# Kernel tuning notes

Measured on AMD Instinct MI355X. Metric: run time of the kernel, lower is better.

Reference implementation:

```python
import jax, jax.numpy as jnp
import numpy as np

N = 100000   # nodes
E = 1600000  # edges
D = 128      # input feature dim
H = 64       # hidden dim
G = 64       # graphs in batch


def setup_inputs() -> dict:
    key = jax.random.key(0)
    ks = jax.random.split(key, 12)
    x = jax.random.normal(ks[0], (N, D), dtype=jnp.float32)
    ei = jax.random.randint(ks[1], (2, E), 0, N, dtype=jnp.int32)
    ew = jax.random.uniform(ks[2], (E,), dtype=jnp.float32)
    b = jnp.sort(jax.random.randint(ks[3], (N,), 0, G, dtype=jnp.int32))
    s = 0.05
    W1 = jax.random.normal(ks[4], (D, H), jnp.float32) * s
    b1 = jnp.zeros((H,), jnp.float32)
    W2 = jax.random.normal(ks[5], (H, H), jnp.float32) * s
    b2 = jnp.zeros((H,), jnp.float32)
    Wm1 = jax.random.normal(ks[6], (H, 32), jnp.float32) * s
    bm1 = jnp.zeros((32,), jnp.float32)
    Wm2 = jax.random.normal(ks[7], (32, 1), jnp.float32) * s
    bm2 = jnp.zeros((1,), jnp.float32)
    return {"x": x, "ei": ei, "ew": ew, "b": b,
            "W1": W1, "b1": b1, "W2": W2, "b2": b2,
            "Wm1": Wm1, "bm1": bm1, "Wm2": Wm2, "bm2": bm2}


def _gcn_norm(ei, ew, n):
    # PyG gcn_norm with add_self_loops=True (self-loop weight 1)
    loops = jnp.arange(n, dtype=ei.dtype)
    row = jnp.concatenate([ei[0], loops])
    col = jnp.concatenate([ei[1], loops])
    w = jnp.concatenate([ew, jnp.ones((n,), ew.dtype)])
    deg = jax.ops.segment_sum(w, col, num_segments=n)
    dinv = jnp.where(deg > 0, jax.lax.rsqrt(deg), 0.0)
    norm = dinv[row] * w * dinv[col]  # [E+N]
    return row, col, norm


def _gcn_conv(x, W, bias, row, col, norm, n):
    h = x @ W                                   # [N,H] small GEMM
    msg = h[row] * norm[:, None]                # gather over edges
    return jax.ops.segment_sum(msg, col, num_segments=n) + bias


def reference(x, ei, ew, b, W1, b1, W2, b2, Wm1, bm1, Wm2, bm2):
    n = x.shape[0]
    row, col, norm = _gcn_norm(ei, ew, n)
    h = jax.nn.relu(_gcn_conv(x, W1, b1, row, col, norm, n))
    h = jax.nn.relu(_gcn_conv(h, W2, b2, row, col, norm, n))
    # global_mean_pool over batch vector b
    sums = jax.ops.segment_sum(h, b, num_segments=G)
    cnt = jax.ops.segment_sum(jnp.ones((n,), h.dtype), b, num_segments=G)
    pooled = sums / jnp.maximum(cnt, 1.0)[:, None]  # [G,H]
    # MLP head: Linear(H,32) -> ReLU -> Linear(32,1)
    return jax.nn.relu(pooled @ Wm1 + bm1) @ Wm2 + bm2
```

## Files before the change

### kernel.cpp

```cpp
#include <hip/hip_runtime.h>
#include <hip/hip_bf16.h>
#include <hip/hip_fp16.h>


#define DIMH 64
#define BSH 7
#define BSZ 128
#define NBUCK_MAX 1024
#define EPB 4096
#define ESTRIDE 3072
#define CSTRIDE 4096

typedef _Float16 v8h __attribute__((ext_vector_type(8)));
typedef _Float16 v4h __attribute__((ext_vector_type(4)));
typedef _Float16 hv2 __attribute__((ext_vector_type(2)));
typedef float v4f __attribute__((ext_vector_type(4)));

__global__ __launch_bounds__(512) void k_part(const int* __restrict__ row,
                                              const int* __restrict__ col,
                                              const float* __restrict__ ew,
                                              int* __restrict__ cursor,
                                              unsigned long long* __restrict__ part,
                                              int E, int nbuck) {
    __shared__ int h[NBUCK_MAX];
    __shared__ int h2[NBUCK_MAX];
    __shared__ int st[NBUCK_MAX];
    for (int i = threadIdx.x; i < nbuck; i += 512) { h[i] = 0; h2[i] = 0; }
    __syncthreads();
    int ebeg = blockIdx.x * EPB;
    int eend = min(ebeg + EPB, E);
    int myc[8];
    int m = 0;
    for (int e = ebeg + threadIdx.x; e < eend; e += 512) {
        int c = col[e];
        myc[m++] = c;
        atomicAdd(&h[c >> BSH], 1);
    }
    __syncthreads();
    for (int i = threadIdx.x; i < nbuck; i += 512) {
        int c = h[i];
        st[i] = c ? i * ESTRIDE + atomicAdd(&cursor[i], c) : 0;
    }
    __syncthreads();
    m = 0;
    for (int e = ebeg + threadIdx.x; e < eend; e += 512, m++) {
        int c = myc[m];
        int b = c >> BSH;
        int r = atomicAdd(&h2[b], 1);
        int slot = st[b] + r;
        if (slot < (b + 1) * ESTRIDE) {
            unsigned long long rec =
                ((unsigned long long)__float_as_uint(ew[e]) << 32) |
                ((unsigned long long)(unsigned)row[e] << 8) |
                (unsigned)(c & (BSZ - 1));
            part[slot] = rec;
        }
    }
}

__global__ __launch_bounds__(256) void k_sortB(const unsigned long long* __restrict__ part,
                                               const int* __restrict__ cursor,
                                               int2* __restrict__ csr,
                                               unsigned* __restrict__ rp,
                                               float* __restrict__ dinv, int N) {
    __shared__ int cnt[BSZ];
    __shared__ int scn[BSZ];
    __shared__ int cur[BSZ];
    __shared__ float dg[BSZ];
    int b = blockIdx.x;
    int nb0 = b << BSH;
    int nn = min(BSZ, N - nb0);
    int tid = threadIdx.x;
    if (tid < BSZ) { cnt[tid] = 0; dg[tid] = 1.0f; }
    __syncthreads();
    int ebeg = b * ESTRIDE;
    int eend = ebeg + min(cursor[b], ESTRIDE);
    unsigned long long myrec[12];
    int nrec = 0;
    for (int e = ebeg + tid; e < eend; e += 256) {
        unsigned long long rec = part[e];
        myrec[nrec++] = rec;
        atomicAdd(&cnt[(int)(rec & (BSZ - 1))], 1);
    }
    __syncthreads();
    int pc = 0;
    if (tid < BSZ) pc = min((cnt[tid] + 7) & ~7, 496);
    if (tid < BSZ) scn[tid] = pc;
    __syncthreads();
    for (int o = 1; o < BSZ; o <<= 1) {
        int t = 0;
        if (tid >= o && tid < BSZ) t = scn[tid - o];
        __syncthreads();
        if (tid >= o && tid < BSZ) scn[tid] += t;
        __syncthreads();
    }
    int Pb = b * CSTRIDE;
    int pofs = 0;
    if (tid < BSZ) {
        pofs = scn[tid] - pc;
        cur[tid] = pofs;
        if (tid < nn)
            rp[nb0 + tid] = ((unsigned)(pc >> 3) << 26) | (unsigned)(Pb + pofs);
    }
    __syncthreads();
    for (int i = 0; i < nrec; i++) {
        unsigned long long rec = myrec[i];
        int cl = (int)(rec & (BSZ - 1));
        float w = __uint_as_float((unsigned)(rec >> 32));
        int slot = atomicAdd(&cur[cl], 1);
        csr[Pb + slot] = make_int2((int)((rec >> 8) & 0xFFFFFF), __float_as_int(w));
        atomicAdd(&dg[cl], w);
    }
    __syncthreads();
    if (tid < nn) {
        int c = min(cnt[tid], pc);
        for (int k = c; k < pc; k++)
            csr[Pb + pofs + k] = make_int2(nb0 + tid, 0);
        dinv[nb0 + tid] = rsqrtf(dg[tid]);
    }
}

__global__ __launch_bounds__(256) void k_gemm_mfma(const float* __restrict__ X,
                                                   const float* __restrict__ W,
                                                   const float* __restrict__ dinv,
                                                   __half* __restrict__ Y, int n) {
    __shared__ _Float16 Wh[128 * 64];
    int tid = threadIdx.x;
    for (int i = tid * 4; i < 128 * 64; i += 256 * 4) {
        float4 w = *(const float4*)&W[i];
        Wh[i]     = (_Float16)w.x;
        Wh[i + 1] = (_Float16)w.y;
        Wh[i + 2] = (_Float16)w.z;
        Wh[i + 3] = (_Float16)w.w;
    }
    __syncthreads();

    int wv = tid >> 6;
    int lane = tid & 63;
    int m = lane & 15;
    int quad = lane >> 4;
    int tile = blockIdx.x * 4 + wv;
    int ntiles = (n + 15) >> 4;
    if (tile >= ntiles) return;

    v8h bf[4][4];
#pragma unroll
    for (int nt = 0; nt < 4; nt++)
#pragma unroll
        for (int s = 0; s < 4; s++)
#pragma unroll
            for (int j = 0; j < 8; j++)
                bf[nt][s][j] = Wh[(s * 32 + quad * 8 + j) * 64 + nt * 16 + m];

    v4f acc[4];
#pragma unroll
    for (int nt = 0; nt < 4; nt++) acc[nt] = (v4f){0.f, 0.f, 0.f, 0.f};

    int row = min(tile * 16 + m, n - 1);
    const float* xr = X + (size_t)row * 128;
#pragma unroll
    for (int s = 0; s < 4; s++) {
        float4 lo = *(const float4*)&xr[s * 32 + quad * 8];
        float4 hi = *(const float4*)&xr[s * 32 + quad * 8 + 4];
        v8h af;
        af[0] = (_Float16)lo.x; af[1] = (_Float16)lo.y;
        af[2] = (_Float16)lo.z; af[3] = (_Float16)lo.w;
        af[4] = (_Float16)hi.x; af[5] = (_Float16)hi.y;
        af[6] = (_Float16)hi.z; af[7] = (_Float16)hi.w;
#pragma unroll
        for (int nt = 0; nt < 4; nt++)
            acc[nt] = __builtin_amdgcn_mfma_f32_16x16x32_f16(af, bf[nt][s], acc[nt], 0, 0, 0);
    }

#pragma unroll
    for (int r = 0; r < 4; r++) {
        int node = tile * 16 + quad * 4 + r;
        if (node < n) {
            float di = dinv[node];
#pragma unroll
            for (int nt = 0; nt < 4; nt++)
                Y[(size_t)node * DIMH + nt * 16 + m] = __float2half(di * acc[nt][r]);
        }
    }
}

__global__ __launch_bounds__(256, 8) void k_agg1f(const __half* __restrict__ Hin,
                                                  const unsigned* __restrict__ rp,
                                                  const int2* __restrict__ csr,
                                                  const float* __restrict__ dinv,
                                                  const float* __restrict__ bias,
                                                  const float* __restrict__ W2,
                                                  __half* __restrict__ T2, int n) {
    __shared__ __align__(16) _Float16 W2T[64 * 68];
    __shared__ __align__(16) _Float16 hbuf[4][DIMH];
    int tid = threadIdx.x;
    for (int idx = tid; idx < 64 * 64; idx += 256) {
        int k = idx >> 6;
        int o = idx & 63;
        W2T[o * 68 + k] = (_Float16)W2[idx];
    }
    __syncthreads();

    int lane = tid & 63;
    int wv = tid >> 6;
    int q = lane >> 4;
    int fp = lane & 15;

    const char* Hb = (const char*)Hin;
    const char* Cb = (const char*)csr;
    int ngroups = (n + 3) >> 2;
    for (int grp = blockIdx.x; grp < ngroups; grp += gridDim.x) {
        int node = grp * 4 + wv;
        if (node >= n) continue;
        unsigned pk = rp[node];
        unsigned pb = ((pk & 0x3FFFFFFu) << 3) + (unsigned)(q << 4);
        int g8 = (int)(pk >> 26);
        float a0 = 0.f, a1 = 0.f, a2 = 0.f, a3 = 0.f;
        if (q == 0) {
            uint2 su = *(const uint2*)(Hb + (((unsigned)node << 7) + (unsigned)(fp << 3)));
            float2 f0 = __half22float2(*(__half2*)&su.x);
            float2 f1 = __half22float2(*(__half2*)&su.y);
            a0 = f0.x; a1 = f0.y; a2 = f1.x; a3 = f1.y;
        }
        unsigned fo = (unsigned)(fp << 3);
        int it = 0;
        for (; it + 4 <= g8; it += 4, pb += 256) {
            int4 mA0 = *(const int4*)(Cb + pb);
            int4 mB0 = *(const int4*)(Cb + pb + 64);
            int4 mA1 = *(const int4*)(Cb + pb + 128);
            int4 mB1 = *(const int4*)(Cb + pb + 192);
            uint2 u0 = *(const uint2*)(Hb + (((unsigned)mA0.x << 7) + fo));
            uint2 u1 = *(const uint2*)(Hb + (((unsigned)mA0.z << 7) + fo));
            uint2 u2 = *(const uint2*)(Hb + (((unsigned)mB0.x << 7) + fo));
            uint2 u3 = *(const uint2*)(Hb + (((unsigned)mB0.z << 7) + fo));
            uint2 u4 = *(const uint2*)(Hb + (((unsigned)mA1.x << 7) + fo));
            uint2 u5 = *(const uint2*)(Hb + (((unsigned)mA1.z << 7) + fo));
            uint2 u6 = *(const uint2*)(Hb + (((unsigned)mB1.x << 7) + fo));
            uint2 u7 = *(const uint2*)(Hb + (((unsigned)mB1.z << 7) + fo));
            float w0 = __int_as_float(mA0.y), w1 = __int_as_float(mA0.w);
            float w2 = __int_as_float(mB0.y), w3 = __int_as_float(mB0.w);
            float w4 = __int_as_float(mA1.y), w5 = __int_as_float(mA1.w);
            float w6 = __int_as_float(mB1.y), w7 = __int_as_float(mB1.w);
            float2 f;
            f = __half22float2(*(__half2*)&u0.x); a0 += w0 * f.x; a1 += w0 * f.y;
            f = __half22float2(*(__half2*)&u0.y); a2 += w0 * f.x; a3 += w0 * f.y;
            f = __half22float2(*(__half2*)&u1.x); a0 += w1 * f.x; a1 += w1 * f.y;
            f = __half22float2(*(__half2*)&u1.y); a2 += w1 * f.x; a3 += w1 * f.y;
            f = __half22float2(*(__half2*)&u2.x); a0 += w2 * f.x; a1 += w2 * f.y;
            f = __half22float2(*(__half2*)&u2.y); a2 += w2 * f.x; a3 += w2 * f.y;
            f = __half22float2(*(__half2*)&u3.x); a0 += w3 * f.x; a1 += w3 * f.y;
            f = __half22float2(*(__half2*)&u3.y); a2 += w3 * f.x; a3 += w3 * f.y;
            f = __half22float2(*(__half2*)&u4.x); a0 += w4 * f.x; a1 += w4 * f.y;
            f = __half22float2(*(__half2*)&u4.y); a2 += w4 * f.x; a3 += w4 * f.y;
            f = __half22float2(*(__half2*)&u5.x); a0 += w5 * f.x; a1 += w5 * f.y;
            f = __half22float2(*(__half2*)&u5.y); a2 += w5 * f.x; a3 += w5 * f.y;
            f = __half22float2(*(__half2*)&u6.x); a0 += w6 * f.x; a1 += w6 * f.y;
            f = __half22float2(*(__half2*)&u6.y); a2 += w6 * f.x; a3 += w6 * f.y;
            f = __half22float2(*(__half2*)&u7.x); a0 += w7 * f.x; a1 += w7 * f.y;
            f = __half22float2(*(__half2*)&u7.y); a2 += w7 * f.x; a3 += w7 * f.y;
        }
        if (it + 2 <= g8) {
            int4 mA = *(const int4*)(Cb + pb);
            int4 mB = *(const int4*)(Cb + pb + 64);
            uint2 u0 = *(const uint2*)(Hb + (((unsigned)mA.x << 7) + fo));
            uint2 u1 = *(const uint2*)(Hb + (((unsigned)mA.z << 7) + fo));
            uint2 u2 = *(const uint2*)(Hb + (((unsigned)mB.x << 7) + fo));
            uint2 u3 = *(const uint2*)(Hb + (((unsigned)mB.z << 7) + fo));
            float w0 = __int_as_float(mA.y), w1 = __int_as_float(mA.w);
            float w2 = __int_as_float(mB.y), w3 = __int_as_float(mB.w);
            float2 f;
            f = __half22float2(*(__half2*)&u0.x); a0 += w0 * f.x; a1 += w0 * f.y;
            f = __half22float2(*(__half2*)&u0.y); a2 += w0 * f.x; a3 += w0 * f.y;
            f = __half22float2(*(__half2*)&u1.x); a0 += w1 * f.x; a1 += w1 * f.y;
            f = __half22float2(*(__half2*)&u1.y); a2 += w1 * f.x; a3 += w1 * f.y;
            f = __half22float2(*(__half2*)&u2.x); a0 += w2 * f.x; a1 += w2 * f.y;
            f = __half22float2(*(__half2*)&u2.y); a2 += w2 * f.x; a3 += w2 * f.y;
            f = __half22float2(*(__half2*)&u3.x); a0 += w3 * f.x; a1 += w3 * f.y;
            f = __half22float2(*(__half2*)&u3.y); a2 += w3 * f.x; a3 += w3 * f.y;
            pb += 128; it += 2;
        }
        if (it < g8) {
            int4 mA = *(const int4*)(Cb + pb);
            uint2 u0 = *(const uint2*)(Hb + (((unsigned)mA.x << 7) + fo));
            uint2 u1 = *(const uint2*)(Hb + (((unsigned)mA.z << 7) + fo));
            float w0 = __int_as_float(mA.y), w1 = __int_as_float(mA.w);
            float2 f;
            f = __half22float2(*(__half2*)&u0.x); a0 += w0 * f.x; a1 += w0 * f.y;
            f = __half22float2(*(__half2*)&u0.y); a2 += w0 * f.x; a3 += w0 * f.y;
            f = __half22float2(*(__half2*)&u1.x); a0 += w1 * f.x; a1 += w1 * f.y;
            f = __half22float2(*(__half2*)&u1.y); a2 += w1 * f.x; a3 += w1 * f.y;
        }
        a0 += __shfl_xor(a0, 16, 64); a0 += __shfl_xor(a0, 32, 64);
        a1 += __shfl_xor(a1, 16, 64); a1 += __shfl_xor(a1, 32, 64);
        a2 += __shfl_xor(a2, 16, 64); a2 += __shfl_xor(a2, 32, 64);
        a3 += __shfl_xor(a3, 16, 64); a3 += __shfl_xor(a3, 32, 64);
        float di = dinv[node];
        if (q == 0) {
            float4 bs = *(const float4*)&bias[fp * 4];
            float v0 = fmaxf(di * a0 + bs.x, 0.f);
            float v1 = fmaxf(di * a1 + bs.y, 0.f);
            float v2 = fmaxf(di * a2 + bs.z, 0.f);
            float v3 = fmaxf(di * a3 + bs.w, 0.f);
            __half2 h0 = __floats2half2_rn(v0, v1);
            __half2 h1 = __floats2half2_rn(v2, v3);
            uint2 o;
            o.x = *(unsigned*)&h0;
            o.y = *(unsigned*)&h1;
            *(uint2*)&hbuf[wv][fp * 4] = o;
        }
        float accA = 0.f, accB = 0.f;
#pragma unroll
        for (int k8 = 0; k8 < 8; k8++) {
            v8h hv = *(const v8h*)&hbuf[wv][k8 * 8];
            v4h wa = *(const v4h*)&W2T[lane * 68 + k8 * 8];
            v4h wb = *(const v4h*)&W2T[lane * 68 + k8 * 8 + 4];
            hv2 h0 = {hv[0], hv[1]}, h1 = {hv[2], hv[3]};
            hv2 h2_ = {hv[4], hv[5]}, h3 = {hv[6], hv[7]};
            hv2 w0 = {wa[0], wa[1]}, w1 = {wa[2], wa[3]};
            hv2 w2_ = {wb[0], wb[1]}, w3 = {wb[2], wb[3]};
            accA = __builtin_amdgcn_fdot2(h0, w0, accA, false);
            accB = __builtin_amdgcn_fdot2(h1, w1, accB, false);
            accA = __builtin_amdgcn_fdot2(h2_, w2_, accA, false);
            accB = __builtin_amdgcn_fdot2(h3, w3, accB, false);
        }
        T2[(size_t)node * DIMH + lane] = __float2half(di * (accA + accB));
    }
}

__global__ __launch_bounds__(256, 8) void k_aggN(const __half* __restrict__ Hin,
                                                 const unsigned* __restrict__ rp,
                                                 const int2* __restrict__ csr,
                                                 const float* __restrict__ dinv,
                                                 const float* __restrict__ bias,
                                                 __half* __restrict__ Hout, int n) {
    int lane = threadIdx.x & 63;
    int wv = threadIdx.x >> 6;
    int node = blockIdx.x * 4 + wv;
    if (node >= n) return;
    unsigned pk = rp[node];
    int g8 = (int)(pk >> 26);
    int q = lane >> 4;
    int fp = lane & 15;
    unsigned pb = ((pk & 0x3FFFFFFu) << 3) + (unsigned)(q << 4);
    unsigned fo = (unsigned)(fp << 3);
    const char* Hb = (const char*)Hin;
    const char* Cb = (const char*)csr;
    float a0 = 0.f, a1 = 0.f, a2 = 0.f, a3 = 0.f;
    if (q == 0) {
        uint2 su = *(const uint2*)(Hb + (((unsigned)node << 7) + fo));
        float2 f0 = __half22float2(*(__half2*)&su.x);
        float2 f1 = __half22float2(*(__half2*)&su.y);
        a0 = f0.x; a1 = f0.y; a2 = f1.x; a3 = f1.y;
    }
    int it = 0;
    for (; it + 4 <= g8; it += 4, pb += 256) {
        int4 mA0 = *(const int4*)(Cb + pb);
        int4 mB0 = *(const int4*)(Cb + pb + 64);
        int4 mA1 = *(const int4*)(Cb + pb + 128);
        int4 mB1 = *(const int4*)(Cb + pb + 192);
        uint2 u0 = *(const uint2*)(Hb + (((unsigned)mA0.x << 7) + fo));
        uint2 u1 = *(const uint2*)(Hb + (((unsigned)mA0.z << 7) + fo));
        uint2 u2 = *(const uint2*)(Hb + (((unsigned)mB0.x << 7) + fo));
        uint2 u3 = *(const uint2*)(Hb + (((unsigned)mB0.z << 7) + fo));
        uint2 u4 = *(const uint2*)(Hb + (((unsigned)mA1.x << 7) + fo));
        uint2 u5 = *(const uint2*)(Hb + (((unsigned)mA1.z << 7) + fo));
        uint2 u6 = *(const uint2*)(Hb + (((unsigned)mB1.x << 7) + fo));
        uint2 u7 = *(const uint2*)(Hb + (((unsigned)mB1.z << 7) + fo));
        float w0 = __int_as_float(mA0.y), w1 = __int_as_float(mA0.w);
        float w2 = __int_as_float(mB0.y), w3 = __int_as_float(mB0.w);
        float w4 = __int_as_float(mA1.y), w5 = __int_as_float(mA1.w);
        float w6 = __int_as_float(mB1.y), w7 = __int_as_float(mB1.w);
        float2 f;
        f = __half22float2(*(__half2*)&u0.x); a0 += w0 * f.x; a1 += w0 * f.y;
        f = __half22float2(*(__half2*)&u0.y); a2 += w0 * f.x; a3 += w0 * f.y;
        f = __half22float2(*(__half2*)&u1.x); a0 += w1 * f.x; a1 += w1 * f.y;
        f = __half22float2(*(__half2*)&u1.y); a2 += w1 * f.x; a3 += w1 * f.y;
        f = __half22float2(*(__half2*)&u2.x); a0 += w2 * f.x; a1 += w2 * f.y;
        f = __half22float2(*(__half2*)&u2.y); a2 += w2 * f.x; a3 += w2 * f.y;
        f = __half22float2(*(__half2*)&u3.x); a0 += w3 * f.x; a1 += w3 * f.y;
        f = __half22float2(*(__half2*)&u3.y); a2 += w3 * f.x; a3 += w3 * f.y;
        f = __half22float2(*(__half2*)&u4.x); a0 += w4 * f.x; a1 += w4 * f.y;
        f = __half22float2(*(__half2*)&u4.y); a2 += w4 * f.x; a3 += w4 * f.y;
        f = __half22float2(*(__half2*)&u5.x); a0 += w5 * f.x; a1 += w5 * f.y;
        f = __half22float2(*(__half2*)&u5.y); a2 += w5 * f.x; a3 += w5 * f.y;
        f = __half22float2(*(__half2*)&u6.x); a0 += w6 * f.x; a1 += w6 * f.y;
        f = __half22float2(*(__half2*)&u6.y); a2 += w6 * f.x; a3 += w6 * f.y;
        f = __half22float2(*(__half2*)&u7.x); a0 += w7 * f.x; a1 += w7 * f.y;
        f = __half22float2(*(__half2*)&u7.y); a2 += w7 * f.x; a3 += w7 * f.y;
    }
    if (it + 2 <= g8) {
        int4 mA = *(const int4*)(Cb + pb);
        int4 mB = *(const int4*)(Cb + pb + 64);
        uint2 u0 = *(const uint2*)(Hb + (((unsigned)mA.x << 7) + fo));
        uint2 u1 = *(const uint2*)(Hb + (((unsigned)mA.z << 7) + fo));
        uint2 u2 = *(const uint2*)(Hb + (((unsigned)mB.x << 7) + fo));
        uint2 u3 = *(const uint2*)(Hb + (((unsigned)mB.z << 7) + fo));
        float w0 = __int_as_float(mA.y), w1 = __int_as_float(mA.w);
        float w2 = __int_as_float(mB.y), w3 = __int_as_float(mB.w);
        float2 f;
        f = __half22float2(*(__half2*)&u0.x); a0 += w0 * f.x; a1 += w0 * f.y;
        f = __half22float2(*(__half2*)&u0.y); a2 += w0 * f.x; a3 += w0 * f.y;
        f = __half22float2(*(__half2*)&u1.x); a0 += w1 * f.x; a1 += w1 * f.y;
        f = __half22float2(*(__half2*)&u1.y); a2 += w1 * f.x; a3 += w1 * f.y;
        f = __half22float2(*(__half2*)&u2.x); a0 += w2 * f.x; a1 += w2 * f.y;
        f = __half22float2(*(__half2*)&u2.y); a2 += w2 * f.x; a3 += w2 * f.y;
        f = __half22float2(*(__half2*)&u3.x); a0 += w3 * f.x; a1 += w3 * f.y;
        f = __half22float2(*(__half2*)&u3.y); a2 += w3 * f.x; a3 += w3 * f.y;
        pb += 128; it += 2;
    }
    if (it < g8) {
        int4 mA = *(const int4*)(Cb + pb);
        uint2 u0 = *(const uint2*)(Hb + (((unsigned)mA.x << 7) + fo));
        uint2 u1 = *(const uint2*)(Hb + (((unsigned)mA.z << 7) + fo));
        float w0 = __int_as_float(mA.y), w1 = __int_as_float(mA.w);
        float2 f;
        f = __half22float2(*(__half2*)&u0.x); a0 += w0 * f.x; a1 += w0 * f.y;
        f = __half22float2(*(__half2*)&u0.y); a2 += w0 * f.x; a3 += w0 * f.y;
        f = __half22float2(*(__half2*)&u1.x); a0 += w1 * f.x; a1 += w1 * f.y;
        f = __half22float2(*(__half2*)&u1.y); a2 += w1 * f.x; a3 += w1 * f.y;
    }
    a0 += __shfl_xor(a0, 16, 64); a0 += __shfl_xor(a0, 32, 64);
    a1 += __shfl_xor(a1, 16, 64); a1 += __shfl_xor(a1, 32, 64);
    a2 += __shfl_xor(a2, 16, 64); a2 += __shfl_xor(a2, 32, 64);
    a3 += __shfl_xor(a3, 16, 64); a3 += __shfl_xor(a3, 32, 64);
    if (q == 0) {
        float di = dinv[node];
        float4 bs = *(const float4*)&bias[fp * 4];
        float v0 = fmaxf(di * a0 + bs.x, 0.f);
        float v1 = fmaxf(di * a1 + bs.y, 0.f);
        float v2 = fmaxf(di * a2 + bs.z, 0.f);
        float v3 = fmaxf(di * a3 + bs.w, 0.f);
        __half2 h0 = __floats2half2_rn(v0, v1);
        __half2 h1 = __floats2half2_rn(v2, v3);
        uint2 o;
        o.x = *(unsigned*)&h0;
        o.y = *(unsigned*)&h1;
        *(uint2*)&Hout[(size_t)node * DIMH + fp * 4] = o;
    }
}

__global__ __launch_bounds__(256) void k_pool(const __half* __restrict__ Hin,
                                              const int* __restrict__ b,
                                              float* __restrict__ sums,
                                              float* __restrict__ cntG, int n) {
    const int CHUNK = 64;
    int lane = threadIdx.x & 63;
    int wave = threadIdx.x >> 6;
    int start = (blockIdx.x * 4 + wave) * CHUNK;
    if (start >= n) return;
    int end = min(start + CHUNK, n);
    float acc = 0.f;
    int g_cur = b[start];
    int cnt_local = 0;
    for (int i = start; i < end; i++) {
        int g = b[i];
        if (g != g_cur) {
            atomicAdd(&sums[g_cur * DIMH + lane], acc);
            if (lane == 0) atomicAdd(&cntG[g_cur], (float)cnt_local);
            acc = 0.f;
            cnt_local = 0;
            g_cur = g;
        }
        acc += __half2float(Hin[(size_t)i * DIMH + lane]);
        cnt_local++;
    }
    atomicAdd(&sums[g_cur * DIMH + lane], acc);
    if (lane == 0) atomicAdd(&cntG[g_cur], (float)cnt_local);
}

__global__ __launch_bounds__(64) void k_mlp(const float* __restrict__ sums,
                                            const float* __restrict__ cntG,
                                            const float* __restrict__ Wm1,
                                            const float* __restrict__ bm1,
                                            const float* __restrict__ Wm2,
                                            const float* __restrict__ bm2,
                                            float* __restrict__ out, int G) {
    int g = threadIdx.x;
    if (g >= G) return;
    float c = cntG[g];
    float inv = 1.f / (c > 1.f ? c : 1.f);
    float pooled[DIMH];
#pragma unroll
    for (int k = 0; k < DIMH; k++) pooled[k] = sums[g * DIMH + k] * inv;
    float o = 0.f;
    for (int j = 0; j < 32; j++) {
        float t = bm1[j];
#pragma unroll
        for (int k = 0; k < DIMH; k++) t += pooled[k] * Wm1[k * 32 + j];
        t = t > 0.f ? t : 0.f;
        o += t * Wm2[j];
    }
    out[g] = o + bm2[0];
}


extern "C" void kernel_launch(void* const* d_in, const int* in_sizes, int n_in,
                              void* d_out, int out_size, void* d_ws, size_t ws_size,
                              hipStream_t stream) {
    const float* x   = (const float*)d_in[0];
    const int*   ei  = (const int*)d_in[1];
    const float* ew  = (const float*)d_in[2];
    const int*   bvec= (const int*)d_in[3];
    const float* W1  = (const float*)d_in[4];
    const float* b1  = (const float*)d_in[5];
    const float* W2  = (const float*)d_in[6];
    const float* b2  = (const float*)d_in[7];
    const float* Wm1 = (const float*)d_in[8];
    const float* bm1 = (const float*)d_in[9];
    const float* Wm2 = (const float*)d_in[10];
    const float* bm2 = (const float*)d_in[11];
    float* out = (float*)d_out;

    const int E = in_sizes[2];
    const int N = in_sizes[3];
    const int G = out_size;
    const int* row = ei;
    const int* col = ei + E;
    const int nbuck = (N + BSZ - 1) >> BSH;

    char* p = (char*)d_ws;
    auto alloc = [&](size_t bytes) {
        void* r = (void*)p;
        p += (bytes + 255) & ~(size_t)255;
        return r;
    };

    unsigned long long* part = (unsigned long long*)alloc((size_t)nbuck * ESTRIDE * 8);
    int2*  csr    = (int2*)alloc((size_t)nbuck * CSTRIDE * 8);
    unsigned* rp  = (unsigned*)alloc((size_t)N * 4);
    float* dinv   = (float*)alloc((size_t)N * 4);
    __half* hA    = (__half*)alloc((size_t)N * DIMH * 2);
    __half* hB    = (__half*)alloc((size_t)N * DIMH * 2);
    int zeroInts  = nbuck + G * DIMH + G;
    int* cursor   = (int*)alloc((size_t)zeroInts * 4);
    float* sums   = (float*)(cursor + nbuck);
    float* cntG   = sums + G * DIMH;

    hipMemsetAsync(cursor, 0, (size_t)zeroInts * 4, stream);

    const int PB = (E + EPB - 1) / EPB;
    const int NT = (N + 15) / 16;

    k_part<<<PB, 512, 0, stream>>>(row, col, ew, cursor, part, E, nbuck);
    k_sortB<<<nbuck, 256, 0, stream>>>(part, cursor, csr, rp, dinv, N);

    k_gemm_mfma<<<(NT + 3) / 4, 256, 0, stream>>>(x, W1, dinv, hA, N);

    k_agg1f<<<4096, 256, 0, stream>>>(hA, rp, csr, dinv, b1, W2, hB, N);

    k_aggN<<<(N + 3) / 4, 256, 0, stream>>>(hB, rp, csr, dinv, b2, hA, N);

    k_pool<<<(N + 255) / 256, 256, 0, stream>>>(hA, bvec, sums, cntG, N);
    k_mlp<<<1, 64, 0, stream>>>(sums, cntG, Wm1, bm1, Wm2, bm2, out, G);
}
```

Measured before the change: 307.1 us.

## Replace bucket-partition CSR build with global atomic count, scan, scatter

The two-pass bucket partition (shared-memory histograms, intermediate 64-bit record buffer, per-bucket local sort) is replaced by three kernels. One counts per-node in-degree and weighted degree with global atomics, one does a per-bucket prefix scan that writes row pointers, dinv and padding, and one scatters edges directly into the CSR using per-node atomic cursors. This drops the intermediate partition buffer and its extra read and write pass. In exchange it adds heavy global atomic traffic on random column indices (two atomics per edge in counting, one per edge in scatter) and makes the in-row edge order nondeterministic.

```diff
diff --git a/kernel.cpp b/kernel.cpp
--- a/kernel.cpp
+++ b/kernel.cpp
@@ -6,9 +6,6 @@
 #define DIMH 64
 #define BSH 7
 #define BSZ 128
-#define NBUCK_MAX 1024
-#define EPB 4096
-#define ESTRIDE 3072
 #define CSTRIDE 4096
 
 typedef _Float16 v8h __attribute__((ext_vector_type(8)));
@@ -16,107 +13,102 @@
 typedef _Float16 hv2 __attribute__((ext_vector_type(2)));
 typedef float v4f __attribute__((ext_vector_type(4)));
 
-__global__ __launch_bounds__(512) void k_part(const int* __restrict__ row,
-                                              const int* __restrict__ col,
-                                              const float* __restrict__ ew,
-                                              int* __restrict__ cursor,
-                                              unsigned long long* __restrict__ part,
-                                              int E, int nbuck) {
-    __shared__ int h[NBUCK_MAX];
-    __shared__ int h2[NBUCK_MAX];
-    __shared__ int st[NBUCK_MAX];
-    for (int i = threadIdx.x; i < nbuck; i += 512) { h[i] = 0; h2[i] = 0; }
-    __syncthreads();
-    int ebeg = blockIdx.x * EPB;
-    int eend = min(ebeg + EPB, E);
-    int myc[8];
-    int m = 0;
-    for (int e = ebeg + threadIdx.x; e < eend; e += 512) {
-        int c = col[e];
-        myc[m++] = c;
-        atomicAdd(&h[c >> BSH], 1);
-    }
-    __syncthreads();
-    for (int i = threadIdx.x; i < nbuck; i += 512) {
-        int c = h[i];
-        st[i] = c ? i * ESTRIDE + atomicAdd(&cursor[i], c) : 0;
-    }
-    __syncthreads();
-    m = 0;
-    for (int e = ebeg + threadIdx.x; e < eend; e += 512, m++) {
-        int c = myc[m];
-        int b = c >> BSH;
-        int r = atomicAdd(&h2[b], 1);
-        int slot = st[b] + r;
-        if (slot < (b + 1) * ESTRIDE) {
-            unsigned long long rec =
-                ((unsigned long long)__float_as_uint(ew[e]) << 32) |
-                ((unsigned long long)(unsigned)row[e] << 8) |
-                (unsigned)(c & (BSZ - 1));
-            part[slot] = rec;
-        }
-    }
-}
-
-__global__ __launch_bounds__(256) void k_sortB(const unsigned long long* __restrict__ part,
-                                               const int* __restrict__ cursor,
-                                               int2* __restrict__ csr,
-                                               unsigned* __restrict__ rp,
-                                               float* __restrict__ dinv, int N) {
-    __shared__ int cnt[BSZ];
+__global__ __launch_bounds__(256) void k_count(const int* __restrict__ col,
+                                               const float* __restrict__ ew,
+                                               int* __restrict__ degcnt,
+                                               float* __restrict__ degw, int E) {
+    int i = blockIdx.x * 256 + threadIdx.x;
+    int stride = gridDim.x * 256;
+    int E4 = E >> 2;
+    for (int e = i; e < E4; e += stride) {
+        int4 c = *(const int4*)&col[e * 4];
+        float4 w = *(const float4*)&ew[e * 4];
+        atomicAdd(&degcnt[c.x], 1); atomicAdd(&degw[c.x], w.x);
+        atomicAdd(&degcnt[c.y], 1); atomicAdd(&degw[c.y], w.y);
+        atomicAdd(&degcnt[c.z], 1); atomicAdd(&degw[c.z], w.z);
+        atomicAdd(&degcnt[c.w], 1); atomicAdd(&degw[c.w], w.w);
+    }
+    for (int e = (E4 << 2) + i; e < E; e += stride) {
+        atomicAdd(&degcnt[col[e]], 1);
+        atomicAdd(&degw[col[e]], ew[e]);
+    }
+}
+
+__global__ __launch_bounds__(128) void k_scan(int* __restrict__ degcnt,
+                                              const float* __restrict__ degw,
+                                              int2* __restrict__ csr,
+                                              unsigned* __restrict__ rp,
+                                              float* __restrict__ dinv, int N) {
     __shared__ int scn[BSZ];
-    __shared__ int cur[BSZ];
-    __shared__ float dg[BSZ];
     int b = blockIdx.x;
-    int nb0 = b << BSH;
-    int nn = min(BSZ, N - nb0);
     int tid = threadIdx.x;
-    if (tid < BSZ) { cnt[tid] = 0; dg[tid] = 1.0f; }
-    __syncthreads();
-    int ebeg = b * ESTRIDE;
-    int eend = ebeg + min(cursor[b], ESTRIDE);
-    unsigned long long myrec[12];
-    int nrec = 0;
-    for (int e = ebeg + tid; e < eend; e += 256) {
-        unsigned long long rec = part[e];
-        myrec[nrec++] = rec;
-        atomicAdd(&cnt[(int)(rec & (BSZ - 1))], 1);
-    }
-    __syncthreads();
-    int pc = 0;
-    if (tid < BSZ) pc = min((cnt[tid] + 7) & ~7, 496);
-    if (tid < BSZ) scn[tid] = pc;
+    int node = (b << BSH) + tid;
+    int deg = node < N ? degcnt[node] : 0;
+    int pc = min((deg + 7) & ~7, 496);
+    scn[tid] = pc;
     __syncthreads();
     for (int o = 1; o < BSZ; o <<= 1) {
         int t = 0;
-        if (tid >= o && tid < BSZ) t = scn[tid - o];
+        if (tid >= o) t = scn[tid - o];
         __syncthreads();
-        if (tid >= o && tid < BSZ) scn[tid] += t;
+        if (tid >= o) scn[tid] += t;
         __syncthreads();
     }
-    int Pb = b * CSTRIDE;
-    int pofs = 0;
-    if (tid < BSZ) {
-        pofs = scn[tid] - pc;
-        cur[tid] = pofs;
-        if (tid < nn)
-            rp[nb0 + tid] = ((unsigned)(pc >> 3) << 26) | (unsigned)(Pb + pofs);
-    }
-    __syncthreads();
-    for (int i = 0; i < nrec; i++) {
-        unsigned long long rec = myrec[i];
-        int cl = (int)(rec & (BSZ - 1));
-        float w = __uint_as_float((unsigned)(rec >> 32));
-        int slot = atomicAdd(&cur[cl], 1);
-        csr[Pb + slot] = make_int2((int)((rec >> 8) & 0xFFFFFF), __float_as_int(w));
-        atomicAdd(&dg[cl], w);
-    }
-    __syncthreads();
-    if (tid < nn) {
-        int c = min(cnt[tid], pc);
-        for (int k = c; k < pc; k++)
-            csr[Pb + pofs + k] = make_int2(nb0 + tid, 0);
-        dinv[nb0 + tid] = rsqrtf(dg[tid]);
+    if (node < N) {
+        int pofs = scn[tid] - pc;
+        int Pb = b * CSTRIDE;
+        rp[node] = ((unsigned)(pc >> 3) << 26) | (unsigned)(Pb + pofs);
+        dinv[node] = rsqrtf(1.0f + degw[node]);
+        degcnt[node] = 0;
+        for (int k = deg; k < pc; k++)
+            csr[Pb + pofs + k] = make_int2(node, 0);
+    }
+}
+
+__global__ __launch_bounds__(256) void k_scatter(const int* __restrict__ row,
+                                                 const int* __restrict__ col,
+                                                 const float* __restrict__ ew,
+                                                 const unsigned* __restrict__ rp,
+                                                 int* __restrict__ cur,
+                                                 int2* __restrict__ csr, int E) {
+    int i = blockIdx.x * 256 + threadIdx.x;
+    int stride = gridDim.x * 256;
+    int E4 = E >> 2;
+    for (int e = i; e < E4; e += stride) {
+        int4 r = *(const int4*)&row[e * 4];
+        int4 c = *(const int4*)&col[e * 4];
+        float4 w = *(const float4*)&ew[e * 4];
+        {
+            unsigned pk = rp[c.x];
+            int s = atomicAdd(&cur[c.x], 1);
+            if (s < (int)((pk >> 26) << 3))
+                csr[(pk & 0x3FFFFFFu) + s] = make_int2(r.x, __float_as_int(w.x));
+        }
+        {
+            unsigned pk = rp[c.y];
+            int s = atomicAdd(&cur[c.y], 1);
+            if (s < (int)((pk >> 26) << 3))
+                csr[(pk & 0x3FFFFFFu) + s] = make_int2(r.y, __float_as_int(w.y));
+        }
+        {
+            unsigned pk = rp[c.z];
+            int s = atomicAdd(&cur[c.z], 1);
+            if (s < (int)((pk >> 26) << 3))
+                csr[(pk & 0x3FFFFFFu) + s] = make_int2(r.z, __float_as_int(w.z));
+        }
+        {
+            unsigned pk = rp[c.w];
+            int s = atomicAdd(&cur[c.w], 1);
+            if (s < (int)((pk >> 26) << 3))
+                csr[(pk & 0x3FFFFFFu) + s] = make_int2(r.w, __float_as_int(w.w));
+        }
+    }
+    for (int e = (E4 << 2) + i; e < E; e += stride) {
+        int c = col[e];
+        unsigned pk = rp[c];
+        int s = atomicAdd(&cur[c], 1);
+        if (s < (int)((pk >> 26) << 3))
+            csr[(pk & 0x3FFFFFFu) + s] = make_int2(row[e], __float_as_int(ew[e]));
     }
 }
 
@@ -525,24 +517,25 @@
         return r;
     };
 
-    unsigned long long* part = (unsigned long long*)alloc((size_t)nbuck * ESTRIDE * 8);
     int2*  csr    = (int2*)alloc((size_t)nbuck * CSTRIDE * 8);
     unsigned* rp  = (unsigned*)alloc((size_t)N * 4);
     float* dinv   = (float*)alloc((size_t)N * 4);
     __half* hA    = (__half*)alloc((size_t)N * DIMH * 2);
     __half* hB    = (__half*)alloc((size_t)N * DIMH * 2);
-    int zeroInts  = nbuck + G * DIMH + G;
-    int* cursor   = (int*)alloc((size_t)zeroInts * 4);
-    float* sums   = (float*)(cursor + nbuck);
-    float* cntG   = sums + G * DIMH;
-
-    hipMemsetAsync(cursor, 0, (size_t)zeroInts * 4, stream);
-
-    const int PB = (E + EPB - 1) / EPB;
+    size_t zeroInts = (size_t)N * 2 + (size_t)G * DIMH + G;
+    int* degcnt   = (int*)alloc(zeroInts * 4);
+    float* degw   = (float*)(degcnt + N);
+    float* sums   = degw + N;
+    float* cntG   = sums + (size_t)G * DIMH;
+
+    hipMemsetAsync(degcnt, 0, zeroInts * 4, stream);
+
     const int NT = (N + 15) / 16;
-
-    k_part<<<PB, 512, 0, stream>>>(row, col, ew, cursor, part, E, nbuck);
-    k_sortB<<<nbuck, 256, 0, stream>>>(part, cursor, csr, rp, dinv, N);
+    const int CB = min((E / 4 + 255) / 256, 4096);
+
+    k_count<<<CB, 256, 0, stream>>>(col, ew, degcnt, degw, E);
+    k_scan<<<nbuck, 128, 0, stream>>>(degcnt, degw, csr, rp, dinv, N);
+    k_scatter<<<CB, 256, 0, stream>>>(row, col, ew, rp, degcnt, csr, E);
 
     k_gemm_mfma<<<(NT + 3) / 4, 256, 0, stream>>>(x, W1, dinv, hA, N);
 
```

After: 510.8 us. 1.66x slower.
